# Kernel tuning notes

Measured on AMD Instinct MI355X. Metric: run time of the kernel, lower is better.

## Reference

```python
import jax, jax.numpy as jnp
import numpy as np

B, T, C = 4, 1024, 2048
NH, HS = 16, 128          # n_head, head_size
NLQ, NLKV = 1536, 512     # q/kv latent dims
DHR = 64                  # rope head dim


def _rope(x, cos, sin):
    # x: [B, T, H, d]; cos/sin: [T, d//2]
    xr = x.reshape(x.shape[:-1] + (-1, 2))
    x_re, x_im = xr[..., 0], xr[..., 1]
    c = cos[None, :, None, :]
    s = sin[None, :, None, :]
    out = jnp.stack([x_re * c - x_im * s, x_re * s + x_im * c], axis=-1)
    return out.reshape(x.shape)


def setup_inputs() -> dict:
    key = jax.random.key(0)
    ks = jax.random.split(key, 10)
    w = 0.02  # init scale
    x = jax.random.normal(ks[0], (B, T, C), dtype=jnp.float32)
    # RoPE frequencies (standard theta=10000)
    inv_freq = 1.0 / (10000.0 ** (np.arange(0, DHR, 2, dtype=np.float32) / DHR))
    t = np.arange(T, dtype=np.float32)
    ang = np.outer(t, inv_freq)  # [T, DHR//2]
    cos = jnp.asarray(np.cos(ang), dtype=jnp.float32)
    sin = jnp.asarray(np.sin(ang), dtype=jnp.float32)
    return {
        "x": x,
        "cos": cos,
        "sin": sin,
        "W_dq": jax.random.normal(ks[1], (NLQ, C), jnp.float32) * w,
        "W_uq": jax.random.normal(ks[2], (C, NLQ), jnp.float32) * w,
        "W_dkv": jax.random.normal(ks[3], (NLKV, C), jnp.float32) * w,
        "W_uk": jax.random.normal(ks[4], (C, NLKV), jnp.float32) * w,
        "W_uv": jax.random.normal(ks[5], (C, NLKV), jnp.float32) * w,
        "W_qr": jax.random.normal(ks[6], (NH * DHR, NLQ), jnp.float32) * w,
        "W_kr": jax.random.normal(ks[7], (DHR, C), jnp.float32) * w,
        "W_o": jax.random.normal(ks[8], (C, C), jnp.float32) * w,
    }


def reference(x, cos, sin, W_dq, W_uq, W_dkv, W_uk, W_uv, W_qr, W_kr, W_o):
    # down-projected query latent: [B, T, NLQ]
    c_q = jnp.einsum('btc,qc->btq', x, W_dq)
    # absorbed matrices (training-path math, identical to inference buffers)
    # W_uq.weight [C, NLQ] viewed flat as (NLQ, NH, HS) then heads first
    k_eff = jnp.einsum('hqd,hdk->hqk',
                       W_uq.reshape(NLQ, NH, HS).transpose(1, 0, 2),
                       W_uk.reshape(NH, HS, NLKV))           # [NH, NLQ, NLKV]
    v_eff = (W_uv.T @ W_o.T).reshape(NLKV, NH, HS).transpose(1, 0, 2)  # [NH, NLKV, HS]
    # kv latent: [B, T, NLKV]
    c_kv = jnp.einsum('btc,kc->btk', x, W_dkv)
    # content scores via absorbed matmuls: [B, NH, T, T]
    q_abs = jnp.einsum('btq,hqk->bhtk', c_q, k_eff)
    attn_c = jnp.einsum('bhtk,bsk->bhts', q_abs, c_kv)
    # decoupled RoPE branch
    c_kr = jnp.einsum('btc,dc->btd', x, W_kr)[:, :, None, :]   # [B,T,1,DHR]
    k_r = _rope(c_kr, cos, sin)[:, :, 0, :]                     # [B,T,DHR]
    c_qr = jnp.einsum('btq,rq->btr', c_q, W_qr).reshape(B, T, NH, DHR)
    q_r = _rope(c_qr, cos, sin)                                 # [B,T,NH,DHR]
    attn_r = jnp.einsum('bthd,bsd->bhts', q_r, k_r)             # [B,NH,T,T]
    attn = (attn_c + attn_r) / jnp.sqrt(jnp.float32(HS + DHR))
    # causal mask
    mask = jnp.tril(jnp.ones((T, T), dtype=bool))
    attn = jnp.where(mask[None, None], attn, jnp.float32(-jnp.inf))
    attn = jax.nn.softmax(attn, axis=-1)
    # output via absorbed value/output projection
    y_lat = jnp.einsum('bhts,bsk->bhtk', attn, c_kv)            # [B,NH,T,NLKV]
    y = jnp.einsum('bhtk,hkd->bthd', y_lat, v_eff).reshape(B, T, C)
    return y
```

## Files before the change

kernel.cpp:

```cpp
#include <hip/hip_runtime.h>
#include <type_traits>

typedef unsigned short ushort_t;
typedef unsigned int   uint_t;
typedef __attribute__((ext_vector_type(8))) short bf16x8;
typedef __attribute__((ext_vector_type(4))) float f32x4;

constexpr int Bn = 4, Tn = 1024, Cn = 2048, NH = 16, HS = 128;
constexpr int NLQ = 1536, NLKV = 512, DHR = 64;
constexpr int BT = Bn * Tn;
constexpr int KLD = 640;
constexpr float ATT_SCALE = 0.07216878364870323f;
constexpr float LOG2E = 1.4426950408889634f;

__device__ __forceinline__ ushort_t f2bf(float f) {
    uint_t u = __float_as_uint(f);
    u += 0x7fffu + ((u >> 16) & 1u);
    return (ushort_t)(u >> 16);
}

__device__ __forceinline__ void gload_lds16(const void* g, void* l) {
    __builtin_amdgcn_global_load_lds(
        (__attribute__((address_space(1))) void*)g,
        (__attribute__((address_space(3))) void*)l, 16, 0, 0);
}

__device__ __forceinline__ void pipe_wait4(bool last) {
    if (last) asm volatile("s_waitcnt vmcnt(0)" ::: "memory");
    else      asm volatile("s_waitcnt vmcnt(4)" ::: "memory");
    __builtin_amdgcn_s_barrier();
    asm volatile("" ::: "memory");
}


template<typename OutT>
__device__ __forceinline__ void gemm_tile128_pipe(
    const ushort_t* __restrict__ Ab, int lda,
    const ushort_t* __restrict__ Bb, int ldb,
    OutT* __restrict__ Cb, int ldc, int K,
    ushort_t* As, ushort_t* Bs)
{
    const int tid  = threadIdx.x;
    const int lane = tid & 63;
    const int w    = tid >> 6;
    const int l15 = lane & 15, l4 = lane >> 4;
    const int wr = w >> 1, wc = w & 1;
    const int srow = lane >> 2;
    const int scolsw = (((lane & 3) ^ ((srow >> 1) & 3)) * 8);
    const int l4s8 = (l4 ^ ((l15 >> 1) & 3)) * 8;
    const int nT = K >> 5;

    auto stage = [&](int t) {
        const int buf = t % 3;
        const int k0 = t * 32;
        #pragma unroll
        for (int i = 0; i < 2; ++i) {
            int r = w * 32 + i * 16;
            gload_lds16(Ab + (long)(r + srow) * lda + k0 + scolsw, &As[buf * 4096 + r * 32]);
            gload_lds16(Bb + (long)(r + srow) * ldb + k0 + scolsw, &Bs[buf * 4096 + r * 32]);
        }
    };

    f32x4 acc[4][4];
    #pragma unroll
    for (int m = 0; m < 4; ++m)
        #pragma unroll
        for (int n = 0; n < 4; ++n) acc[m][n] = (f32x4){0.f, 0.f, 0.f, 0.f};

    stage(0);
    if (nT > 1) stage(1);

    for (int t = 0; t < nT; ++t) {
        pipe_wait4(t + 1 >= nT);
        if (t + 2 < nT) stage(t + 2);
        const int buf = t % 3;

        bf16x8 af[4], bfv[4];
        #pragma unroll
        for (int m = 0; m < 4; ++m)
            af[m] = *(const bf16x8*)&As[buf * 4096 + (wr * 64 + m * 16 + l15) * 32 + l4s8];
        #pragma unroll
        for (int n = 0; n < 4; ++n)
            bfv[n] = *(const bf16x8*)&Bs[buf * 4096 + (wc * 64 + n * 16 + l15) * 32 + l4s8];
        #pragma unroll
        for (int m = 0; m < 4; ++m)
            #pragma unroll
            for (int n = 0; n < 4; ++n)
                acc[m][n] = __builtin_amdgcn_mfma_f32_16x16x32_bf16(af[m], bfv[n], acc[m][n], 0, 0, 0);
    }

    #pragma unroll
    for (int m = 0; m < 4; ++m)
        #pragma unroll
        for (int j = 0; j < 4; ++j) {
            long row = wr * 64 + m * 16 + l4 * 4 + j;
            #pragma unroll
            for (int n = 0; n < 4; ++n) {
                long col = wc * 64 + n * 16 + l15;
                if constexpr (std::is_same<OutT, float>::value)
                    Cb[row * ldc + col] = acc[m][n][j];
                else
                    Cb[row * ldc + col] = f2bf(acc[m][n][j]);
            }
        }
}

__global__ __launch_bounds__(256, 2) void g1_mt(
    const ushort_t* __restrict__ xb, const ushort_t* __restrict__ WB1,
    ushort_t* __restrict__ cq_b, ushort_t* __restrict__ kfull,
    const ushort_t* __restrict__ Wo_b, const ushort_t* __restrict__ WuvT_b,
    ushort_t* __restrict__ Mtb)
{
    __shared__ ushort_t As[3 * 4096];
    __shared__ ushort_t Bs[3 * 4096];
    const int id = blockIdx.x;
    if (id < 544) {
        const int sid = (id & 7) * 68 + (id >> 3);
        const int nt = sid % 17, mt = sid / 17;
        const ushort_t* Ab = xb + (long)mt * 128 * Cn;
        const ushort_t* Bb = WB1 + (long)nt * 128 * Cn;
        ushort_t* Cb; int ldc;
        if (nt < 12) { Cb = cq_b + (long)mt * 128 * NLQ + nt * 128;          ldc = NLQ; }
        else         { Cb = kfull + (long)mt * 128 * KLD + (nt - 12) * 128;  ldc = KLD; }
        gemm_tile128_pipe<ushort_t>(Ab, Cn, Bb, Cn, Cb, ldc, Cn, As, Bs);
    } else {
        const int local = id - 544;
        const int mt = local >> 2, nt = local & 3;
        const ushort_t* Ab = Wo_b + (long)mt * 128 * Cn;
        const ushort_t* Bb = WuvT_b + (long)nt * 128 * Cn;
        ushort_t* Cb = Mtb + (long)mt * 128 * NLKV + nt * 128;
        gemm_tile128_pipe<ushort_t>(Ab, Cn, Bb, Cn, Cb, NLKV, Cn, As, Bs);
    }
}

__global__ __launch_bounds__(256, 2) void g2_ropekr(
    const ushort_t* __restrict__ cq_b, const ushort_t* __restrict__ WB2,
    ushort_t* __restrict__ qnom, ushort_t* __restrict__ qr_b,
    ushort_t* __restrict__ kfull,
    const float* __restrict__ cosT, const float* __restrict__ sinT)
{
    __shared__ ushort_t As[3 * 4096];
    __shared__ ushort_t Bs[3 * 4096];
    const int id = blockIdx.x;
    if (id < 768) {
        const int sid = (id & 7) * 96 + (id >> 3);
        const int nt = sid % 24, mt = sid / 24;
        const ushort_t* Ab = cq_b + (long)mt * 128 * NLQ;
        const ushort_t* Bb = WB2 + (long)nt * 128 * NLQ;
        ushort_t* Cb; int ldc;
        if (nt < 16) { Cb = qnom + (long)mt * 128 * Cn + nt * 128;               ldc = Cn; }
        else         { Cb = qr_b + (long)mt * 128 * (NH*DHR) + (nt - 16) * 128;  ldc = NH*DHR; }
        gemm_tile128_pipe<ushort_t>(Ab, NLQ, Bb, NLQ, Cb, ldc, NLQ, As, Bs);
    } else {
        int p = (id - 768) * 256 + threadIdx.x;
        if (p >= BT * 32) return;
        int bt = p >> 5, i = p & 31;
        int t = bt & (Tn - 1);
        float c = cosT[t * 32 + i], s = sinT[t * 32 + i];
        uint_t u = *(const uint_t*)&kfull[(long)bt * KLD + 512 + 2 * i];
        float re = __uint_as_float(u << 16);
        float im = __uint_as_float(u & 0xffff0000u);
        float o0 = re * c - im * s, o1 = re * s + im * c;
        uint_t o = (uint_t)f2bf(o0) | ((uint_t)f2bf(o1) << 16);
        *(uint_t*)&kfull[(long)bt * KLD + 512 + 2 * i] = o;
    }
}

__global__ __launch_bounds__(256, 2) void g3_ropeqr(
    const ushort_t* __restrict__ kfull, const ushort_t* __restrict__ WB3,
    ushort_t* __restrict__ kabs, ushort_t* __restrict__ Veff,
    ushort_t* __restrict__ qr_b,
    const float* __restrict__ cosT, const float* __restrict__ sinT)
{
    __shared__ ushort_t As[3 * 4096];
    __shared__ ushort_t Bs[3 * 4096];
    const int id = blockIdx.x;
    if (id < 1024) {
        const int sid = (id & 7) * 128 + (id >> 3);
        const int nt = sid % 32, mt = sid / 32;
        const ushort_t* Ab = kfull + (long)mt * 128 * KLD;
        const ushort_t* Bb = WB3 + (long)nt * 128 * NLKV;
        ushort_t* Cb; long coff;
        if (nt < 16) { Cb = kabs; coff = nt * 128; }
        else         { Cb = Veff; coff = (nt - 16) * 128; }
        gemm_tile128_pipe<ushort_t>(Ab, KLD, Bb, NLKV,
                                    Cb + (long)mt * 128 * Cn + coff, Cn, NLKV, As, Bs);
    } else {
        int p = (id - 1024) * 256 + threadIdx.x;
        if (p >= BT * 512) return;
        int bt = p >> 9, rem = p & 511;
        int hh = rem >> 5, i = rem & 31;
        int t = bt & (Tn - 1);
        float c = cosT[t * 32 + i], s = sinT[t * 32 + i];
        long off = (long)bt * 1024 + hh * 64 + 2 * i;
        uint_t u = *(const uint_t*)&qr_b[off];
        float re = __uint_as_float(u << 16);
        float im = __uint_as_float(u & 0xffff0000u);
        float o0 = re * c - im * s, o1 = re * s + im * c;
        uint_t o = (uint_t)f2bf(o0) | ((uint_t)f2bf(o1) << 16);
        *(uint_t*)&qr_b[off] = o;
    }
}

__global__ __launch_bounds__(256, 2) void attn_s_tv(
    const ushort_t* __restrict__ qnom, const ushort_t* __restrict__ qrb,
    const ushort_t* __restrict__ kabs, const ushort_t* __restrict__ kfull,
    ushort_t* __restrict__ Spk,
    const ushort_t* __restrict__ Veff, ushort_t* __restrict__ VeffT)
{
    __shared__ ushort_t As[3 * 4096];
    __shared__ ushort_t Bs[3 * 4096];
    const int id = blockIdx.x;
    if (id >= 2304) {
        int idx = (id - 2304) * 256 + threadIdx.x;
        int c = idx & 2047, rest = idx >> 11;
        int t8 = rest & 127, b = rest >> 7;
        ushort_t v[8];
        #pragma unroll
        for (int j = 0; j < 8; ++j)
            v[j] = Veff[((long)b * Tn + t8 * 8 + j) * 2048 + c];
        *(uint4*)&VeffT[((long)b * 2048 + c) * Tn + t8 * 8] = *(const uint4*)v;
        return;
    }
    const int sid = (id & 7) * 288 + (id >> 3);
    const int x = sid % 36, z = sid / 36;
    int ti = 0;
    while ((ti + 1) * (ti + 2) / 2 <= x) ++ti;
    const int si = x - ti * (ti + 1) / 2;
    const int h = z >> 2, b = z & 3;

    const int tid  = threadIdx.x;
    const int lane = tid & 63;
    const int w    = tid >> 6;
    const int l15 = lane & 15, l4 = lane >> 4;
    const int wr = w >> 1, wc = w & 1;
    const int srow = lane >> 2;
    const int scolsw = (((lane & 3) ^ ((srow >> 1) & 3)) * 8);
    const int l4s8 = (l4 ^ ((l15 >> 1) & 3)) * 8;

    const ushort_t* A1 = qnom + ((long)(b * 1024 + ti * 128)) * 2048 + h * 128;
    const ushort_t* A2 = qrb  + ((long)(b * 1024 + ti * 128)) * 1024 + h * 64;
    const ushort_t* B1 = kabs + ((long)(b * 1024 + si * 128)) * 2048 + h * 128;
    const ushort_t* B2 = kfull + ((long)(b * 1024 + si * 128)) * KLD + 512;
    ushort_t* Cb = Spk + (long)z * 589824 + (long)x * 16384;

    auto stage = [&](int t) {
        const int buf = t % 3;
        const ushort_t* Asrc; const ushort_t* Bsrc; int ldA, ldB;
        if (t < 4) { Asrc = A1 + t * 32;       Bsrc = B1 + t * 32;       ldA = 2048; ldB = 2048; }
        else       { Asrc = A2 + (t - 4) * 32; Bsrc = B2 + (t - 4) * 32; ldA = 1024; ldB = KLD; }
        #pragma unroll
        for (int i = 0; i < 2; ++i) {
            int r = w * 32 + i * 16;
            gload_lds16(Asrc + (long)(r + srow) * ldA + scolsw, &As[buf * 4096 + r * 32]);
            gload_lds16(Bsrc + (long)(r + srow) * ldB + scolsw, &Bs[buf * 4096 + r * 32]);
        }
    };

    f32x4 acc[4][4];
    #pragma unroll
    for (int m = 0; m < 4; ++m)
        #pragma unroll
        for (int n = 0; n < 4; ++n) acc[m][n] = (f32x4){0.f, 0.f, 0.f, 0.f};

    stage(0); stage(1);
    #pragma unroll
    for (int t = 0; t < 6; ++t) {
        pipe_wait4(t == 5);
        if (t + 2 < 6) stage(t + 2);
        const int buf = t % 3;
        bf16x8 af[4], bfv[4];
        #pragma unroll
        for (int m = 0; m < 4; ++m)
            af[m] = *(const bf16x8*)&As[buf * 4096 + (wr * 64 + m * 16 + l15) * 32 + l4s8];
        #pragma unroll
        for (int n = 0; n < 4; ++n)
            bfv[n] = *(const bf16x8*)&Bs[buf * 4096 + (wc * 64 + n * 16 + l15) * 32 + l4s8];
        #pragma unroll
        for (int m = 0; m < 4; ++m)
            #pragma unroll
            for (int n = 0; n < 4; ++n)
                acc[m][n] = __builtin_amdgcn_mfma_f32_16x16x32_bf16(af[m], bfv[n], acc[m][n], 0, 0, 0);
    }

    #pragma unroll
    for (int m = 0; m < 4; ++m)
        #pragma unroll
        for (int j = 0; j < 4; ++j) {
            long row = wr * 64 + m * 16 + l4 * 4 + j;
            #pragma unroll
            for (int n = 0; n < 4; ++n)
                Cb[row * 128 + wc * 64 + n * 16 + l15] = f2bf(acc[m][n][j]);
        }
}

__global__ __launch_bounds__(256) void attn_softmax(ushort_t* __restrict__ Spk)
{
    const int wid  = threadIdx.x >> 6;
    const int lane = threadIdx.x & 63;
    const int r = blockIdx.x * 4 + wid;
    const int z = r >> 10, t = r & 1023;
    const int ti = t >> 7;
    const int nc = ti + 1;
    ushort_t* base = Spk + (long)z * 589824 + (long)(ti * (ti + 1) / 2) * 16384
                        + (t & 127) * 128;
    const float SCL = ATT_SCALE * LOG2E;

    float p0[8], p1[8];
    float mx = -INFINITY;
    #pragma unroll
    for (int c = 0; c < 8; ++c) {
        p0[c] = -INFINITY; p1[c] = -INFINITY;
        if (c < nc) {
            uint_t u = *(const uint_t*)&base[c * 16384 + lane * 2];
            int kv = c * 128 + lane * 2;
            float a  = __uint_as_float(u << 16);
            float bb = __uint_as_float(u & 0xffff0000u);
            if (kv     <= t) p0[c] = a  * SCL;
            if (kv + 1 <= t) p1[c] = bb * SCL;
            mx = fmaxf(mx, fmaxf(p0[c], p1[c]));
        }
    }
    #pragma unroll
    for (int off = 32; off >= 1; off >>= 1) mx = fmaxf(mx, __shfl_xor(mx, off));
    float s = 0.f;
    #pragma unroll
    for (int c = 0; c < 8; ++c) {
        p0[c] = exp2f(p0[c] - mx);
        p1[c] = exp2f(p1[c] - mx);
        if (c < nc) s += p0[c] + p1[c];
    }
    #pragma unroll
    for (int off = 32; off >= 1; off >>= 1) s += __shfl_xor(s, off);
    const float inv = 1.f / s;
    #pragma unroll
    for (int c = 0; c < 8; ++c) if (c < nc) {
        uint_t o = (uint_t)f2bf(p0[c] * inv) | ((uint_t)f2bf(p1[c] * inv) << 16);
        *(uint_t*)&base[c * 16384 + lane * 2] = o;
    }
}

__global__ __launch_bounds__(256, 2) void attn_pv_gemm(
    const ushort_t* __restrict__ Spk, const ushort_t* __restrict__ VeffT,
    float* __restrict__ out)
{
    __shared__ ushort_t As[3 * 4096];
    __shared__ ushort_t Bs[3 * 4096];
    const int id  = blockIdx.x;
    const int sid = (id & 7) * 64 + (id >> 3);
    const int ti = sid & 7, z = sid >> 3;
    const int tid  = threadIdx.x;
    const int lane = tid & 63;
    const int w    = tid >> 6;
    const int l15 = lane & 15, l4 = lane >> 4;
    const int wr = w >> 1, wc = w & 1;
    const int srow = lane >> 2;
    const int scolsw = (((lane & 3) ^ ((srow >> 1) & 3)) * 8);
    const int l4s8 = (l4 ^ ((l15 >> 1) & 3)) * 8;
    const int h = z >> 2, b = z & 3;
    const int nT = (ti + 1) * 4;
    const ushort_t* Abase = Spk + (long)z * 589824 + (long)(ti * (ti + 1) / 2) * 16384;
    const ushort_t* Bb = VeffT + ((long)b * 2048 + h * 128) * 1024;
    float* Cb = out + ((long)b * 1024 + ti * 128) * 2048 + h * 128;

    auto stage = [&](int t) {
        const int buf = t % 3;
        const int k0 = t * 32;
        const ushort_t* At = Abase + (k0 >> 7) * 16384 + (k0 & 127);
        #pragma unroll
        for (int i = 0; i < 2; ++i) {
            int r = w * 32 + i * 16;
            gload_lds16(At + (long)(r + srow) * 128 + scolsw, &As[buf * 4096 + r * 32]);
            gload_lds16(Bb + (long)(r + srow) * 1024 + k0 + scolsw, &Bs[buf * 4096 + r * 32]);
        }
    };

    f32x4 acc[4][4];
    #pragma unroll
    for (int m = 0; m < 4; ++m)
        #pragma unroll
        for (int n = 0; n < 4; ++n) acc[m][n] = (f32x4){0.f, 0.f, 0.f, 0.f};

    stage(0); stage(1);
    for (int t = 0; t < nT; ++t) {
        pipe_wait4(t + 1 >= nT);
        if (t + 2 < nT) stage(t + 2);
        const int buf = t % 3;
        bf16x8 af[4], bfv[4];
        #pragma unroll
        for (int m = 0; m < 4; ++m)
            af[m] = *(const bf16x8*)&As[buf * 4096 + (wr * 64 + m * 16 + l15) * 32 + l4s8];
        #pragma unroll
        for (int n = 0; n < 4; ++n)
            bfv[n] = *(const bf16x8*)&Bs[buf * 4096 + (wc * 64 + n * 16 + l15) * 32 + l4s8];
        #pragma unroll
        for (int m = 0; m < 4; ++m)
            #pragma unroll
            for (int n = 0; n < 4; ++n)
                acc[m][n] = __builtin_amdgcn_mfma_f32_16x16x32_bf16(af[m], bfv[n], acc[m][n], 0, 0, 0);
    }

    #pragma unroll
    for (int m = 0; m < 4; ++m)
        #pragma unroll
        for (int j = 0; j < 4; ++j) {
            long row = wr * 64 + m * 16 + l4 * 4 + j;
            #pragma unroll
            for (int n = 0; n < 4; ++n)
                Cb[row * 2048 + wc * 64 + n * 16 + l15] = acc[m][n][j];
        }
}

__global__ __launch_bounds__(256) void prep_all(
    const float* __restrict__ x,    const float* __restrict__ Wdq,
    const float* __restrict__ Wdkv, const float* __restrict__ Wkr,
    const float* __restrict__ Wqr,  const float* __restrict__ Wo,
    const float* __restrict__ Wuk,  const float* __restrict__ Wuq,
    const float* __restrict__ Wuv,
    ushort_t* __restrict__ xb, ushort_t* __restrict__ WB1,
    ushort_t* __restrict__ WB2, ushort_t* __restrict__ Wo_b,
    ushort_t* __restrict__ WB3, ushort_t* __restrict__ WuvT_b)
{
    const int bid = blockIdx.x;
    const int t = threadIdx.x;

    if (bid >= 9600) {
        __shared__ float tile[64][65];
        const float* in; ushort_t* outp; int ldin, R, c0, r0;
        if (bid < 10368) { int l = bid - 9600;  in = Wuq; outp = WB2;    ldin = 2048; R = 1536; c0 = (l % 32) * 64; r0 = (l / 32) * 64; }
        else             { int l = bid - 10368; in = Wuv; outp = WuvT_b; ldin = 512;  R = 2048; c0 = (l % 8) * 64;  r0 = (l / 8) * 64; }
        #pragma unroll
        for (int i = 0; i < 4; ++i) {
            int idx = t + i * 256;
            int r = idx >> 4, c4 = idx & 15;
            float4 v = *(const float4*)&in[(long)(r0 + r) * ldin + c0 + c4 * 4];
            tile[r][c4 * 4 + 0] = v.x; tile[r][c4 * 4 + 1] = v.y;
            tile[r][c4 * 4 + 2] = v.z; tile[r][c4 * 4 + 3] = v.w;
        }
        __syncthreads();
        #pragma unroll
        for (int i = 0; i < 4; ++i) {
            int idx = t + i * 256;
            int c = idx >> 4, r4 = idx & 15;
            ushort_t p[4];
            #pragma unroll
            for (int j = 0; j < 4; ++j) p[j] = f2bf(tile[r4 * 4 + j][c]);
            *(uint2*)&outp[(long)(c0 + c) * R + r0 + r4 * 4] = *(const uint2*)p;
        }
        return;
    }

    const float* src = nullptr; ushort_t* dst;
    if      (bid < 4096) { src = x    + (long)bid * 2048;          dst = xb   + (long)bid * 2048; }
    else if (bid < 5632) { long b = bid - 4096; src = Wdq  + b * 2048; dst = WB1 + b * 2048; }
    else if (bid < 6144) { long b = bid - 5632; src = Wdkv + b * 2048; dst = WB1 + 3145728 + b * 2048; }
    else if (bid < 6208) { long b = bid - 6144; src = Wkr  + b * 2048; dst = WB1 + 4194304 + b * 2048; }
    else if (bid < 6272) { long b = bid - 6208;                        dst = WB1 + 4325376 + b * 2048; }
    else if (bid < 7040) { long b = bid - 6272; src = Wqr  + b * 2048; dst = WB2 + 3145728 + b * 2048; }
    else if (bid < 9088) { long b = bid - 7040; src = Wo   + b * 2048; dst = Wo_b + b * 2048; }
    else                 { long b = bid - 9088; src = Wuk  + b * 2048; dst = WB3 + b * 2048; }

    const long i = (long)t * 8;
    if (!src) { *(uint4*)&dst[i] = make_uint4(0, 0, 0, 0); return; }
    float4 a = *(const float4*)&src[i];
    float4 b4 = *(const float4*)&src[i + 4];
    ushort_t p[8] = {f2bf(a.x), f2bf(a.y), f2bf(a.z), f2bf(a.w),
                     f2bf(b4.x), f2bf(b4.y), f2bf(b4.z), f2bf(b4.w)};
    *(uint4*)&dst[i] = *(const uint4*)p;
}

extern "C" void kernel_launch(void* const* d_in, const int* in_sizes, int n_in,
                              void* d_out, int out_size, void* d_ws, size_t ws_size,
                              hipStream_t stream)
{
    (void)in_sizes; (void)n_in; (void)out_size; (void)ws_size;
    const float* x     = (const float*)d_in[0];
    const float* cosT  = (const float*)d_in[1];
    const float* sinT  = (const float*)d_in[2];
    const float* W_dq  = (const float*)d_in[3];
    const float* W_uq  = (const float*)d_in[4];
    const float* W_dkv = (const float*)d_in[5];
    const float* W_uk  = (const float*)d_in[6];
    const float* W_uv  = (const float*)d_in[7];
    const float* W_qr  = (const float*)d_in[8];
    const float* W_kr  = (const float*)d_in[9];
    const float* W_o   = (const float*)d_in[10];
    float* out = (float*)d_out;

    ushort_t* ws = (ushort_t*)d_ws;
    ushort_t* xb     = ws;
    ushort_t* WB1    = ws + 8388608;
    ushort_t* WB2    = ws + 12845056;
    ushort_t* Wo_b   = ws + 17563648;
    ushort_t* WuvT_b = ws + 21757952;
    ushort_t* cq_b   = ws + 22806528;
    ushort_t* WB3    = ws + 29097984;
    ushort_t* Spk    = ws;
    ushort_t* qnom   = ws + 39583744;
    ushort_t* qr_b   = ws + 47972352;
    ushort_t* kabs   = ws + 52166656;
    ushort_t* kfull  = ws + 60555264;
    ushort_t* VeffT  = ws + 63176704;
    ushort_t* Veff   = ws + 71565312;
    ushort_t* Mtb    = WB3 + 1048576;

    dim3 blk(256, 1, 1);

    prep_all<<<dim3(10624), blk, 0, stream>>>(
        x, W_dq, W_dkv, W_kr, W_qr, W_o, W_uk, W_uq, W_uv,
        xb, WB1, WB2, Wo_b, WB3, WuvT_b);

    g1_mt<<<dim3(608), blk, 0, stream>>>(xb, WB1, cq_b, kfull, Wo_b, WuvT_b, Mtb);

    g2_ropekr<<<dim3(1280), blk, 0, stream>>>(cq_b, WB2, qnom, qr_b, kfull, cosT, sinT);

    g3_ropeqr<<<dim3(9216), blk, 0, stream>>>(kfull, WB3, kabs, Veff, qr_b, cosT, sinT);

    attn_s_tv<<<dim3(6400), blk, 0, stream>>>(qnom, qr_b, kabs, kfull, Spk, Veff, VeffT);

    attn_softmax<<<dim3(BT * NH / 4), blk, 0, stream>>>(Spk);

    attn_pv_gemm<<<dim3(512), blk, 0, stream>>>(Spk, VeffT, out);
}
```

Baseline: 270.5 us.

## Fuse RoPE into GEMM epilogues and softmax into PV GEMM, merge launches

RoPE for k_r and q_r is applied directly in the GEMM epilogues using lane shuffles, so the separate elementwise RoPE passes go away. The two middle GEMMs are merged into one launch. The softmax kernel is folded into the start of the PV GEMM: each block normalizes its own rows in place before loading them. This removes two extra read/write passes over intermediates and several launches. The cost is a serialized softmax prologue inside each PV block, with only 512 blocks, which may hurt latency hiding.

```diff
diff --git a/kernel.cpp b/kernel.cpp
--- a/kernel.cpp
+++ b/kernel.cpp
@@ -33,12 +33,10 @@
 }
 
 
-template<typename OutT>
-__device__ __forceinline__ void gemm_tile128_pipe(
+__device__ __forceinline__ void gemm_acc_pipe(
     const ushort_t* __restrict__ Ab, int lda,
-    const ushort_t* __restrict__ Bb, int ldb,
-    OutT* __restrict__ Cb, int ldc, int K,
-    ushort_t* As, ushort_t* Bs)
+    const ushort_t* __restrict__ Bb, int ldb, int K,
+    ushort_t* As, ushort_t* Bs, f32x4 (&acc)[4][4])
 {
     const int tid  = threadIdx.x;
     const int lane = tid & 63;
@@ -61,7 +59,6 @@
         }
     };
 
-    f32x4 acc[4][4];
     #pragma unroll
     for (int m = 0; m < 4; ++m)
         #pragma unroll
@@ -74,7 +71,6 @@
         pipe_wait4(t + 1 >= nT);
         if (t + 2 < nT) stage(t + 2);
         const int buf = t % 3;
-
         bf16x8 af[4], bfv[4];
         #pragma unroll
         for (int m = 0; m < 4; ++m)
@@ -88,20 +84,21 @@
             for (int n = 0; n < 4; ++n)
                 acc[m][n] = __builtin_amdgcn_mfma_f32_16x16x32_bf16(af[m], bfv[n], acc[m][n], 0, 0, 0);
     }
-
+}
+
+__device__ __forceinline__ void epi_bf16(f32x4 (&acc)[4][4], ushort_t* Cb, int ldc) {
+    const int lane = threadIdx.x & 63;
+    const int w    = threadIdx.x >> 6;
+    const int l15 = lane & 15, l4 = lane >> 4;
+    const int wr = w >> 1, wc = w & 1;
     #pragma unroll
     for (int m = 0; m < 4; ++m)
         #pragma unroll
         for (int j = 0; j < 4; ++j) {
             long row = wr * 64 + m * 16 + l4 * 4 + j;
             #pragma unroll
-            for (int n = 0; n < 4; ++n) {
-                long col = wc * 64 + n * 16 + l15;
-                if constexpr (std::is_same<OutT, float>::value)
-                    Cb[row * ldc + col] = acc[m][n][j];
-                else
-                    Cb[row * ldc + col] = f2bf(acc[m][n][j]);
-            }
+            for (int n = 0; n < 4; ++n)
+                Cb[row * ldc + wc * 64 + n * 16 + l15] = f2bf(acc[m][n][j]);
         }
 }
 
@@ -109,96 +106,108 @@
     const ushort_t* __restrict__ xb, const ushort_t* __restrict__ WB1,
     ushort_t* __restrict__ cq_b, ushort_t* __restrict__ kfull,
     const ushort_t* __restrict__ Wo_b, const ushort_t* __restrict__ WuvT_b,
-    ushort_t* __restrict__ Mtb)
+    ushort_t* __restrict__ Mtb,
+    const float* __restrict__ cosT, const float* __restrict__ sinT)
 {
     __shared__ ushort_t As[3 * 4096];
     __shared__ ushort_t Bs[3 * 4096];
+    f32x4 acc[4][4];
     const int id = blockIdx.x;
+    const int lane = threadIdx.x & 63;
+    const int w    = threadIdx.x >> 6;
+    const int l15 = lane & 15, l4 = lane >> 4;
+    const int wr = w >> 1, wc = w & 1;
+
     if (id < 544) {
         const int sid = (id & 7) * 68 + (id >> 3);
         const int nt = sid % 17, mt = sid / 17;
-        const ushort_t* Ab = xb + (long)mt * 128 * Cn;
-        const ushort_t* Bb = WB1 + (long)nt * 128 * Cn;
-        ushort_t* Cb; int ldc;
-        if (nt < 12) { Cb = cq_b + (long)mt * 128 * NLQ + nt * 128;          ldc = NLQ; }
-        else         { Cb = kfull + (long)mt * 128 * KLD + (nt - 12) * 128;  ldc = KLD; }
-        gemm_tile128_pipe<ushort_t>(Ab, Cn, Bb, Cn, Cb, ldc, Cn, As, Bs);
+        gemm_acc_pipe(xb + (long)mt * 128 * Cn, Cn, WB1 + (long)nt * 128 * Cn, Cn, Cn,
+                      As, Bs, acc);
+        if (nt < 12) {
+            epi_bf16(acc, cq_b + (long)mt * 128 * NLQ + nt * 128, NLQ);
+        } else if (nt < 16 || wc == 1) {
+            ushort_t* Cb = kfull + (long)mt * 128 * KLD + (nt - 12) * 128;
+            epi_bf16(acc, Cb, KLD);
+        } else {
+            ushort_t* Cb = kfull + (long)mt * 128 * KLD + 512;
+            #pragma unroll
+            for (int m = 0; m < 4; ++m)
+                #pragma unroll
+                for (int j = 0; j < 4; ++j) {
+                    long rowl = wr * 64 + m * 16 + l4 * 4 + j;
+                    int t = (int)((mt * 128 + rowl) & 1023);
+                    #pragma unroll
+                    for (int n = 0; n < 4; ++n) {
+                        float v = acc[m][n][j];
+                        float vr = __shfl_xor(v, 1);
+                        int col = n * 16 + l15;
+                        int i = col >> 1;
+                        float c = cosT[t * 32 + i], s = sinT[t * 32 + i];
+                        float o = ((l15 & 1) == 0) ? (v * c - vr * s) : (vr * s + v * c);
+                        Cb[rowl * KLD + col] = f2bf(o);
+                    }
+                }
+        }
     } else {
         const int local = id - 544;
         const int mt = local >> 2, nt = local & 3;
-        const ushort_t* Ab = Wo_b + (long)mt * 128 * Cn;
-        const ushort_t* Bb = WuvT_b + (long)nt * 128 * Cn;
-        ushort_t* Cb = Mtb + (long)mt * 128 * NLKV + nt * 128;
-        gemm_tile128_pipe<ushort_t>(Ab, Cn, Bb, Cn, Cb, NLKV, Cn, As, Bs);
-    }
-}
-
-__global__ __launch_bounds__(256, 2) void g2_ropekr(
+        gemm_acc_pipe(Wo_b + (long)mt * 128 * Cn, Cn, WuvT_b + (long)nt * 128 * Cn, Cn, Cn,
+                      As, Bs, acc);
+        epi_bf16(acc, Mtb + (long)mt * 128 * NLKV + nt * 128, NLKV);
+    }
+}
+
+__global__ __launch_bounds__(256, 2) void g23(
     const ushort_t* __restrict__ cq_b, const ushort_t* __restrict__ WB2,
     ushort_t* __restrict__ qnom, ushort_t* __restrict__ qr_b,
-    ushort_t* __restrict__ kfull,
+    const ushort_t* __restrict__ kfull, const ushort_t* __restrict__ WB3,
+    ushort_t* __restrict__ kabs, ushort_t* __restrict__ Veff,
     const float* __restrict__ cosT, const float* __restrict__ sinT)
 {
     __shared__ ushort_t As[3 * 4096];
     __shared__ ushort_t Bs[3 * 4096];
+    f32x4 acc[4][4];
     const int id = blockIdx.x;
+    const int lane = threadIdx.x & 63;
+    const int w    = threadIdx.x >> 6;
+    const int l15 = lane & 15, l4 = lane >> 4;
+    const int wr = w >> 1, wc = w & 1;
+
     if (id < 768) {
         const int sid = (id & 7) * 96 + (id >> 3);
         const int nt = sid % 24, mt = sid / 24;
-        const ushort_t* Ab = cq_b + (long)mt * 128 * NLQ;
-        const ushort_t* Bb = WB2 + (long)nt * 128 * NLQ;
-        ushort_t* Cb; int ldc;
-        if (nt < 16) { Cb = qnom + (long)mt * 128 * Cn + nt * 128;               ldc = Cn; }
-        else         { Cb = qr_b + (long)mt * 128 * (NH*DHR) + (nt - 16) * 128;  ldc = NH*DHR; }
-        gemm_tile128_pipe<ushort_t>(Ab, NLQ, Bb, NLQ, Cb, ldc, NLQ, As, Bs);
+        gemm_acc_pipe(cq_b + (long)mt * 128 * NLQ, NLQ, WB2 + (long)nt * 128 * NLQ, NLQ, NLQ,
+                      As, Bs, acc);
+        if (nt < 16) {
+            epi_bf16(acc, qnom + (long)mt * 128 * Cn + nt * 128, Cn);
+        } else {
+            ushort_t* Cb = qr_b + (long)mt * 128 * (NH * DHR) + (nt - 16) * 128;
+            #pragma unroll
+            for (int m = 0; m < 4; ++m)
+                #pragma unroll
+                for (int j = 0; j < 4; ++j) {
+                    long rowl = wr * 64 + m * 16 + l4 * 4 + j;
+                    int t = (int)((mt * 128 + rowl) & 1023);
+                    #pragma unroll
+                    for (int n = 0; n < 4; ++n) {
+                        float v = acc[m][n][j];
+                        float vr = __shfl_xor(v, 1);
+                        int colg = (nt - 16) * 128 + wc * 64 + n * 16 + l15;
+                        int i = (colg & 63) >> 1;
+                        float c = cosT[t * 32 + i], s = sinT[t * 32 + i];
+                        float o = ((l15 & 1) == 0) ? (v * c - vr * s) : (vr * s + v * c);
+                        Cb[rowl * (NH * DHR) + wc * 64 + n * 16 + l15] = f2bf(o);
+                    }
+                }
+        }
     } else {
-        int p = (id - 768) * 256 + threadIdx.x;
-        if (p >= BT * 32) return;
-        int bt = p >> 5, i = p & 31;
-        int t = bt & (Tn - 1);
-        float c = cosT[t * 32 + i], s = sinT[t * 32 + i];
-        uint_t u = *(const uint_t*)&kfull[(long)bt * KLD + 512 + 2 * i];
-        float re = __uint_as_float(u << 16);
-        float im = __uint_as_float(u & 0xffff0000u);
-        float o0 = re * c - im * s, o1 = re * s + im * c;
-        uint_t o = (uint_t)f2bf(o0) | ((uint_t)f2bf(o1) << 16);
-        *(uint_t*)&kfull[(long)bt * KLD + 512 + 2 * i] = o;
-    }
-}
-
-__global__ __launch_bounds__(256, 2) void g3_ropeqr(
-    const ushort_t* __restrict__ kfull, const ushort_t* __restrict__ WB3,
-    ushort_t* __restrict__ kabs, ushort_t* __restrict__ Veff,
-    ushort_t* __restrict__ qr_b,
-    const float* __restrict__ cosT, const float* __restrict__ sinT)
-{
-    __shared__ ushort_t As[3 * 4096];
-    __shared__ ushort_t Bs[3 * 4096];
-    const int id = blockIdx.x;
-    if (id < 1024) {
-        const int sid = (id & 7) * 128 + (id >> 3);
+        const int local = id - 768;
+        const int sid = (local & 7) * 128 + (local >> 3);
         const int nt = sid % 32, mt = sid / 32;
-        const ushort_t* Ab = kfull + (long)mt * 128 * KLD;
-        const ushort_t* Bb = WB3 + (long)nt * 128 * NLKV;
-        ushort_t* Cb; long coff;
-        if (nt < 16) { Cb = kabs; coff = nt * 128; }
-        else         { Cb = Veff; coff = (nt - 16) * 128; }
-        gemm_tile128_pipe<ushort_t>(Ab, KLD, Bb, NLKV,
-                                    Cb + (long)mt * 128 * Cn + coff, Cn, NLKV, As, Bs);
-    } else {
-        int p = (id - 1024) * 256 + threadIdx.x;
-        if (p >= BT * 512) return;
-        int bt = p >> 9, rem = p & 511;
-        int hh = rem >> 5, i = rem & 31;
-        int t = bt & (Tn - 1);
-        float c = cosT[t * 32 + i], s = sinT[t * 32 + i];
-        long off = (long)bt * 1024 + hh * 64 + 2 * i;
-        uint_t u = *(const uint_t*)&qr_b[off];
-        float re = __uint_as_float(u << 16);
-        float im = __uint_as_float(u & 0xffff0000u);
-        float o0 = re * c - im * s, o1 = re * s + im * c;
-        uint_t o = (uint_t)f2bf(o0) | ((uint_t)f2bf(o1) << 16);
-        *(uint_t*)&qr_b[off] = o;
+        gemm_acc_pipe(kfull + (long)mt * 128 * KLD, KLD, WB3 + (long)nt * 128 * NLKV, NLKV, NLKV,
+                      As, Bs, acc);
+        if (nt < 16) epi_bf16(acc, kabs + (long)mt * 128 * Cn + nt * 128, Cn);
+        else         epi_bf16(acc, Veff + (long)mt * 128 * Cn + (nt - 16) * 128, Cn);
     }
 }
 
@@ -294,54 +303,8 @@
         }
 }
 
-__global__ __launch_bounds__(256) void attn_softmax(ushort_t* __restrict__ Spk)
-{
-    const int wid  = threadIdx.x >> 6;
-    const int lane = threadIdx.x & 63;
-    const int r = blockIdx.x * 4 + wid;
-    const int z = r >> 10, t = r & 1023;
-    const int ti = t >> 7;
-    const int nc = ti + 1;
-    ushort_t* base = Spk + (long)z * 589824 + (long)(ti * (ti + 1) / 2) * 16384
-                        + (t & 127) * 128;
-    const float SCL = ATT_SCALE * LOG2E;
-
-    float p0[8], p1[8];
-    float mx = -INFINITY;
-    #pragma unroll
-    for (int c = 0; c < 8; ++c) {
-        p0[c] = -INFINITY; p1[c] = -INFINITY;
-        if (c < nc) {
-            uint_t u = *(const uint_t*)&base[c * 16384 + lane * 2];
-            int kv = c * 128 + lane * 2;
-            float a  = __uint_as_float(u << 16);
-            float bb = __uint_as_float(u & 0xffff0000u);
-            if (kv     <= t) p0[c] = a  * SCL;
-            if (kv + 1 <= t) p1[c] = bb * SCL;
-            mx = fmaxf(mx, fmaxf(p0[c], p1[c]));
-        }
-    }
-    #pragma unroll
-    for (int off = 32; off >= 1; off >>= 1) mx = fmaxf(mx, __shfl_xor(mx, off));
-    float s = 0.f;
-    #pragma unroll
-    for (int c = 0; c < 8; ++c) {
-        p0[c] = exp2f(p0[c] - mx);
-        p1[c] = exp2f(p1[c] - mx);
-        if (c < nc) s += p0[c] + p1[c];
-    }
-    #pragma unroll
-    for (int off = 32; off >= 1; off >>= 1) s += __shfl_xor(s, off);
-    const float inv = 1.f / s;
-    #pragma unroll
-    for (int c = 0; c < 8; ++c) if (c < nc) {
-        uint_t o = (uint_t)f2bf(p0[c] * inv) | ((uint_t)f2bf(p1[c] * inv) << 16);
-        *(uint_t*)&base[c * 16384 + lane * 2] = o;
-    }
-}
-
-__global__ __launch_bounds__(256, 2) void attn_pv_gemm(
-    const ushort_t* __restrict__ Spk, const ushort_t* __restrict__ VeffT,
+__global__ __launch_bounds__(256, 2) void attn_pv_sm(
+    ushort_t* __restrict__ Spk, const ushort_t* __restrict__ VeffT,
     float* __restrict__ out)
 {
     __shared__ ushort_t As[3 * 4096];
@@ -359,14 +322,59 @@
     const int l4s8 = (l4 ^ ((l15 >> 1) & 3)) * 8;
     const int h = z >> 2, b = z & 3;
     const int nT = (ti + 1) * 4;
-    const ushort_t* Abase = Spk + (long)z * 589824 + (long)(ti * (ti + 1) / 2) * 16384;
+    ushort_t* Az = Spk + (long)z * 589824 + (long)(ti * (ti + 1) / 2) * 16384;
+
+    {
+        const int nc = ti + 1;
+        const float SCL = ATT_SCALE * LOG2E;
+        for (int r_i = 0; r_i < 32; ++r_i) {
+            const int rloc = w * 32 + r_i;
+            const int t = ti * 128 + rloc;
+            ushort_t* rowb = Az + rloc * 128 + lane * 2;
+            float p0[8], p1[8];
+            float mx = -INFINITY;
+            #pragma unroll
+            for (int c = 0; c < 8; ++c) {
+                p0[c] = -INFINITY; p1[c] = -INFINITY;
+                if (c < nc) {
+                    uint_t u = *(const uint_t*)&rowb[c * 16384];
+                    int kv = c * 128 + lane * 2;
+                    float a  = __uint_as_float(u << 16);
+                    float bb = __uint_as_float(u & 0xffff0000u);
+                    if (kv     <= t) p0[c] = a  * SCL;
+                    if (kv + 1 <= t) p1[c] = bb * SCL;
+                    mx = fmaxf(mx, fmaxf(p0[c], p1[c]));
+                }
+            }
+            #pragma unroll
+            for (int off = 32; off >= 1; off >>= 1) mx = fmaxf(mx, __shfl_xor(mx, off));
+            float s = 0.f;
+            #pragma unroll
+            for (int c = 0; c < 8; ++c) {
+                p0[c] = exp2f(p0[c] - mx);
+                p1[c] = exp2f(p1[c] - mx);
+                if (c < nc) s += p0[c] + p1[c];
+            }
+            #pragma unroll
+            for (int off = 32; off >= 1; off >>= 1) s += __shfl_xor(s, off);
+            const float inv = 1.f / s;
+            #pragma unroll
+            for (int c = 0; c < 8; ++c) if (c < nc) {
+                uint_t o = (uint_t)f2bf(p0[c] * inv) | ((uint_t)f2bf(p1[c] * inv) << 16);
+                *(uint_t*)&rowb[c * 16384] = o;
+            }
+        }
+    }
+    asm volatile("s_waitcnt vmcnt(0)" ::: "memory");
+    __syncthreads();
+
     const ushort_t* Bb = VeffT + ((long)b * 2048 + h * 128) * 1024;
     float* Cb = out + ((long)b * 1024 + ti * 128) * 2048 + h * 128;
 
     auto stage = [&](int t) {
         const int buf = t % 3;
         const int k0 = t * 32;
-        const ushort_t* At = Abase + (k0 >> 7) * 16384 + (k0 & 127);
+        const ushort_t* At = Az + (k0 >> 7) * 16384 + (k0 & 127);
         #pragma unroll
         for (int i = 0; i < 2; ++i) {
             int r = w * 32 + i * 16;
@@ -510,15 +518,13 @@
         x, W_dq, W_dkv, W_kr, W_qr, W_o, W_uk, W_uq, W_uv,
         xb, WB1, WB2, Wo_b, WB3, WuvT_b);
 
-    g1_mt<<<dim3(608), blk, 0, stream>>>(xb, WB1, cq_b, kfull, Wo_b, WuvT_b, Mtb);
-
-    g2_ropekr<<<dim3(1280), blk, 0, stream>>>(cq_b, WB2, qnom, qr_b, kfull, cosT, sinT);
-
-    g3_ropeqr<<<dim3(9216), blk, 0, stream>>>(kfull, WB3, kabs, Veff, qr_b, cosT, sinT);
+    g1_mt<<<dim3(608), blk, 0, stream>>>(xb, WB1, cq_b, kfull, Wo_b, WuvT_b, Mtb,
+                                         cosT, sinT);
+
+    g23<<<dim3(1792), blk, 0, stream>>>(cq_b, WB2, qnom, qr_b, kfull, WB3,
+                                        kabs, Veff, cosT, sinT);
 
     attn_s_tv<<<dim3(6400), blk, 0, stream>>>(qnom, qr_b, kabs, kfull, Spk, Veff, VeffT);
 
-    attn_softmax<<<dim3(BT * NH / 4), blk, 0, stream>>>(Spk);
-
-    attn_pv_gemm<<<dim3(512), blk, 0, stream>>>(Spk, VeffT, out);
-}
+    attn_pv_sm<<<dim3(512), blk, 0, stream>>>(Spk, VeffT, out);
+}
```

Measured after the change: 359.1 us. 1.33x slower.
